# Kernel tuning notes

Hardware: AMD Instinct MI355X
Metric: run time of the kernel (lower is better)

Reference implementation:

```python
import jax, jax.numpy as jnp
import numpy as np

STRIDE = (4, 4)
MASK = (17, 17)
G_MEAN = 85.384
G_STD = 53.798
LEV = 5  # len(bins)
EPS = 1e-8
_BINS = np.array([0.0, 0.5, G_MEAN - G_STD, G_MEAN, G_MEAN + G_STD], dtype=np.float32)
_DISTS = [1, 2, 4]
_THETAS = [0.0, np.pi / 4, np.pi / 2, 3 * np.pi / 4]
# skimage greycomatrix offsets: (row, col) = (round(sin(t)*d), round(cos(t)*d)), dist-major
OFFSETS = [(int(round(np.sin(t) * d)), int(round(np.cos(t) * d))) for d in _DISTS for t in _THETAS]


def setup_inputs():
    key = jax.random.key(0)
    x = jax.random.uniform(key, (8, 1, 512, 512), dtype=jnp.float32) * 255.0
    return {"inputs": x}


def _sliding_windows(x):
    B, C, H, W = x.shape
    nx = (H - MASK[0]) // STRIDE[0] + 1
    ny = (W - MASK[1]) // STRIDE[1] + 1
    rows = (jnp.arange(nx) * STRIDE[0])[:, None] + jnp.arange(MASK[0])  # (nx, Mx)
    cols = (jnp.arange(ny) * STRIDE[1])[:, None] + jnp.arange(MASK[1])  # (ny, My)
    w = x[:, :, rows]              # (B, C, nx, Mx, W)
    w = w[:, :, :, :, cols]        # (B, C, nx, Mx, ny, My)
    return jnp.transpose(w, (0, 1, 2, 4, 3, 5))  # (B, C, nx, ny, Mx, My)


def _statistics(w):
    m = w.mean(axis=(-2, -1))
    s = w.std(axis=(-2, -1))
    mx = w.max(axis=(-2, -1))
    mn = w.min(axis=(-2, -1))
    # Faithful to original: mean is rescaled in-place BEFORE being used in max/min stats
    m = m / G_MEAN
    s = s / G_STD
    mx = (mx - m) / G_STD
    mn = (m - mn) / G_STD
    return jnp.concatenate([m, s, mx, mn], axis=1)  # (B, 4*C, nx, ny)


def _glcm(qf, dr, dc):
    # qf: (Wn, Mx, My) int32 -> normalized symmetric GLCM (Wn, LEV, LEV)
    Mx, My = qf.shape[-2:]
    if dc >= 0:
        a = qf[:, :Mx - dr, :My - dc]
        b = qf[:, dr:, dc:]
    else:
        a = qf[:, :Mx - dr, -dc:]
        b = qf[:, dr:, :My + dc]
    Wn = qf.shape[0]
    code = (a * LEV + b).reshape(Wn, -1)
    flat = (jnp.arange(Wn, dtype=jnp.int32)[:, None] * (LEV * LEV) + code).reshape(-1)
    cnt = jax.ops.segment_sum(jnp.ones(flat.shape, jnp.float32), flat, num_segments=Wn * LEV * LEV)
    G = cnt.reshape(Wn, LEV, LEV)
    G = G + jnp.swapaxes(G, -1, -2)  # symmetric=True
    return G / jnp.sum(G, axis=(-2, -1), keepdims=True)  # normed=True


def _hist_glcm_features(q):
    # q: (B, C, nx, ny, Mx, My) int32 -> (B, 64, nx, ny) (C must be 1)
    B, C, nx, ny, Mx, My = q.shape
    qf = q.reshape(-1, Mx, My)
    Wn = qf.shape[0]
    G = jnp.stack([_glcm(qf, dr, dc) for dr, dc in OFFSETS], axis=1)  # (Wn, 12, L, L)

    I = jnp.arange(LEV, dtype=jnp.float32)
    d2 = (I[:, None] - I[None, :]) ** 2
    contrast = jnp.einsum('wkij,ij->wk', G, d2)
    homogeneity = jnp.einsum('wkij,ij->wk', G, 1.0 / (1.0 + d2))
    energy = jnp.sqrt(jnp.sum(G * G, axis=(-2, -1)))
    Pi = G.sum(axis=-1)   # (Wn, 12, L)
    Pj = G.sum(axis=-2)
    mu_i = jnp.sum(I * Pi, axis=-1)
    mu_j = jnp.sum(I * Pj, axis=-1)
    di = I[None, None, :] - mu_i[..., None]
    dj = I[None, None, :] - mu_j[..., None]
    std_i = jnp.sqrt(jnp.sum(Pi * di * di, axis=-1))
    std_j = jnp.sqrt(jnp.sum(Pj * dj * dj, axis=-1))
    cov = jnp.einsum('wkij,wki,wkj->wk', G, di, dj)
    denom = std_i * std_j
    correlation = jnp.where(denom < 1e-15, 1.0, cov / jnp.maximum(denom, 1e-30))
    entropy = -jnp.sum(G * jnp.log2(G + EPS), axis=(-2, -1))  # (Wn, 12)

    qv = qf.reshape(Wn, -1)
    cnts = jnp.stack([jnp.sum(qv == k, axis=-1) for k in range(1, LEV)], axis=-1).astype(jnp.float32)
    tot = cnts.sum(axis=-1, keepdims=True)
    hist = jnp.where(tot > 0, cnts / jnp.maximum(tot, 1.0), 0.0)  # (Wn, LEV-1)

    feat = jnp.concatenate([hist, contrast, homogeneity, energy, correlation, entropy], axis=-1)
    feat = feat.reshape(B, C, nx, ny, -1)
    return jnp.transpose(feat, (0, 4, 2, 3, 1))[..., 0]  # (B, 64, nx, ny)


def reference(inputs):
    w = _sliding_windows(inputs)                                   # (B,C,nx,ny,17,17)
    stat = _statistics(w)                                          # (B,4,nx,ny)
    q = (jnp.digitize(w, jnp.asarray(_BINS)) - 1).astype(jnp.int32)
    hg = _hist_glcm_features(q)                                    # (B,64,nx,ny)
    feats = jnp.concatenate([stat, hg], axis=1)                    # (B,68,nx,ny)
    return jnp.mean(feats, axis=(-2, -1))                          # (B,68)
```

## Files before the change

kernel.cpp:

```cpp
#include <hip/hip_runtime.h>


#define G_MEAN_F 85.384f
#define G_STD_F  53.798f
#define MASK_WS_BYTES (8u * 512u * 36u * 8u)

__device__ constexpr int LO15[15] = {0,0,0,0,0,1,1,1,1,2,2,2,3,3,4};
__device__ constexpr int HI15[15] = {0,1,2,3,4,1,2,3,4,2,3,4,3,4,4};

__device__ __forceinline__ float wred(float v) {
#pragma unroll
  for (int m = 32; m; m >>= 1) v += __shfl_xor(v, m, 64);
  return v;
}

__device__ __forceinline__ void load_row(const unsigned long long* mrow, int ly4, unsigned m[5]) {
  unsigned long long a = mrow[0], b = mrow[1], c = mrow[2], d = mrow[3];
  m[1] = (unsigned)(a >> ly4) & 0x1FFFFu;
  m[2] = (unsigned)(b >> ly4) & 0x1FFFFu;
  m[3] = (unsigned)(c >> ly4) & 0x1FFFFu;
  m[4] = (unsigned)(d >> ly4) & 0x1FFFFu;
  m[0] = 0x1FFFFu & ~(m[1] | m[2] | m[3] | m[4]);
}

__device__ __forceinline__ void upd(unsigned cnt[15], const unsigned a[5], const unsigned b[5]) {
#pragma unroll
  for (int u = 0; u < 15; ++u) {
    const int i = LO15[u], j = HI15[u];
    unsigned t = a[i] & b[j];
    if (i != j) t |= a[j] & b[i];
    cnt[u] += __popc(t);
  }
}

template<int DR, int DC>
__device__ __forceinline__ void row_pair(unsigned cnt[15], const unsigned long long* mk,
                                         int row, int ly4) {
  unsigned a[5], b[5];
  load_row(mk + row * 5, ly4, a);
  if (DR > 0) load_row(mk + (row + DR) * 5, ly4, b);
  unsigned as[5], bs[5];
#pragma unroll
  for (int v = 0; v < 5; ++v) {
    unsigned bb = (DR > 0) ? b[v] : a[v];
    as[v] = (DC < 0) ? (a[v] >> (-DC)) : a[v];
    bs[v] = (DC > 0) ? (bb >> DC) : bb;
  }
  upd(cnt, as, bs);
}

__device__ __forceinline__ void feat5(const unsigned cnt[15], float Np,
                                      float& con, float& hom, float& ene,
                                      float& corr, float& ent) {
  const float invN = 1.0f / Np;
  const float inv2N = 0.5f / Np;
  con = 0.0f; hom = 0.0f; ent = 0.0f;
  float eac = 0.0f;
  float P[5] = {0, 0, 0, 0, 0};
#pragma unroll
  for (int u = 0; u < 15; ++u) {
    const int lo = LO15[u], hi = HI15[u];
    const float m = (float)cnt[u];
    const float d2 = (float)((hi - lo) * (hi - lo));
    con += m * d2;
    hom += m * (1.0f / (1.0f + d2));
    if (lo == hi) {
      eac += m * m;
      P[lo] += 2.0f * m;
      float g = m * invN;
      ent -= g * __log2f(g + 1e-8f);
    } else {
      eac += 0.5f * m * m;
      P[lo] += m; P[hi] += m;
      float g = m * inv2N;
      ent -= 2.0f * g * __log2f(g + 1e-8f);
    }
  }
  con *= invN;
  hom *= invN;
  ene = sqrtf(eac) * invN;
  float mu = 0.0f;
#pragma unroll
  for (int i = 0; i < 5; ++i) { P[i] *= inv2N; mu += (float)i * P[i]; }
  float s2 = 0.0f;
#pragma unroll
  for (int i = 0; i < 5; ++i) { float d = (float)i - mu; s2 = fmaf(P[i] * d, d, s2); }
  float denom = s2;
  float cov = 0.0f;
#pragma unroll
  for (int u = 0; u < 15; ++u)
    cov += ((float)cnt[u] * invN) * ((float)LO15[u] - mu) * ((float)HI15[u] - mu);
  corr = (denom < 1e-15f) ? 1.0f : cov / fmaxf(denom, 1e-30f);
}

__device__ __forceinline__ void emit2(const unsigned c1[15], const unsigned c2[15], float Np,
                                      bool v1, bool v2, float* pt0, int k0, int k1) {
  float con1, hom1, ene1, cor1, ent1, con2, hom2, ene2, cor2, ent2;
  feat5(c1, Np, con1, hom1, ene1, cor1, ent1);
  feat5(c2, Np, con2, hom2, ene2, cor2, ent2);
  if (!v1) { con1 = 0; hom1 = 0; ene1 = 0; cor1 = 0; ent1 = 0; }
  if (!v2) { con2 = 0; hom2 = 0; ene2 = 0; cor2 = 0; ent2 = 0; }
  float con = wred(con1 + con2), hom = wred(hom1 + hom2), ene = wred(ene1 + ene2);
  float cor = wred(cor1 + cor2), ent = wred(ent1 + ent2);
  if ((threadIdx.x & 63) == 0) {
    const float s = 1.0f / 15376.0f;
    pt0[(8 + k0) * 128] = con * s;
    pt0[(20 + k0) * 128] = hom * s;
    pt0[(32 + k0) * 128] = ene * s;
    pt0[(44 + k0) * 128] = cor * s;
    pt0[(56 + k0) * 128] = ent * s;
    if (k1 >= 0) {
      pt0[(8 + k1) * 128] = con * s;
      pt0[(20 + k1) * 128] = hom * s;
      pt0[(32 + k1) * 128] = ene * s;
      pt0[(44 + k1) * 128] = cor * s;
      pt0[(56 + k1) * 128] = ent * s;
    }
  }
}

template<int DR, int DC>
__device__ __forceinline__ void glcm_pass(const unsigned long long* mk, int s, int ly4,
                                          float Np, bool v1, bool v2, float* pt0,
                                          int k0, int k1) {
  unsigned A[15], S[15], B[15];
#pragma unroll
  for (int u = 0; u < 15; ++u) { A[u] = 0; S[u] = 0; B[u] = 0; }
#pragma unroll 1
  for (int R = 0; R < 4; ++R) row_pair<DR, DC>(A, mk, s + R, ly4);
#pragma unroll 1
  for (int R = 4; R < 17 - DR; ++R) row_pair<DR, DC>(S, mk, s + R, ly4);
#pragma unroll 1
  for (int R = 17 - DR; R < 21 - DR; ++R) row_pair<DR, DC>(B, mk, s + R, ly4);
#pragma unroll
  for (int u = 0; u < 15; ++u) { A[u] += S[u]; B[u] += S[u]; }
  emit2(A, B, Np, v1, v2, pt0, k0, k1);
}

__global__ __launch_bounds__(64)
void mask_build_kernel(const float* __restrict__ x, unsigned long long* __restrict__ mg) {
  const int lane = threadIdx.x;
  const int r = blockIdx.x;
  const int b = blockIdx.y;
  const float* xr = x + ((size_t)b * 512 + r) * 512;
  unsigned long long* mr = mg + ((size_t)b * 512 + r) * 36;

  const float T1 = 0.5f;
  const float T2 = (float)(85.384 - 53.798);
  const float T3 = 85.384f;
  const float T4 = (float)(85.384 + 53.798);

#pragma unroll 1
  for (int seg = 0; seg < 8; ++seg) {
    float xv = xr[seg * 64 + lane];
    int q = (int)(xv >= T1) + (int)(xv >= T2) + (int)(xv >= T3) + (int)(xv >= T4);
    unsigned long long b1 = __ballot(q == 1);
    unsigned long long b2 = __ballot(q == 2);
    unsigned long long b3 = __ballot(q == 3);
    unsigned long long b4 = __ballot(q == 4);
    if (lane < 4) {
      unsigned long long bv = (lane == 0) ? b1 : (lane == 1) ? b2 : (lane == 2) ? b3 : b4;
      mr[seg * 4 + lane] = bv;
    }
  }
  if (lane < 4) mr[32 + lane] = 0;
}

__global__ __launch_bounds__(128)
void glcm_feat_kernel(const float* __restrict__ x,
                      const unsigned long long* __restrict__ mg,
                      float* __restrict__ part) {
  __shared__ unsigned long long masks[77 * 5];

  const int tid = threadIdx.x;
  const int lane = tid & 63;
  const int wid = tid >> 6;
  const int role = blockIdx.x >> 4;
  const int ty = blockIdx.x & 15;
  const int tx = blockIdx.y;
  const int b = blockIdx.z;
  const int px0 = tx * 64;
  const int py0 = ty * 32;
  const float* xb = x + (size_t)b * 512 * 512;

  const int s0 = py0 >> 6;
  const int sh = py0 & 63;
  const unsigned long long* mgb = mg + (size_t)b * 512 * 36;
#pragma unroll 1
  for (int t = tid; t < 77 * 4; t += 128) {
    int row = t >> 2, lev = t & 3;
    int gr = px0 + row; if (gr > 511) gr = 511;
    const unsigned long long* p = mgb + (size_t)gr * 36 + s0 * 4 + lev;
    unsigned long long w0 = p[0];
    unsigned long long w1 = p[4];
    masks[row * 5 + lev] = sh ? ((w0 >> 32) | (w1 << 32)) : w0;
  }
  __syncthreads();

  const int lxp = lane >> 3, ly = lane & 7;
  const int wx1 = tx * 16 + 2 * lxp;
  const int wy = ty * 8 + ly;
  const bool vy = (wy < 124);
  const bool v1 = (wx1 < 124) && vy;
  const bool v2 = (wx1 + 1 < 124) && vy;
  const int s = 8 * lxp;
  const int ly4 = ly * 4;
  const int tile = tx * 16 + ty;
  float* pt0 = part + (size_t)b * 68 * 128 + tile;

  if (role == 0) {
    if (wid == 0) {
      unsigned hA[4] = {0,0,0,0}, hS[4] = {0,0,0,0}, hB[4] = {0,0,0,0};
#pragma unroll 1
      for (int R = 0; R < 21; ++R) {
        unsigned m[5];
        load_row(masks + (s + R) * 5, ly4, m);
        unsigned* h = (R < 4) ? hA : (R < 17) ? hS : hB;
#pragma unroll
        for (int v = 0; v < 4; ++v) h[v] += __popc(m[v + 1]);
      }
      int sp = px0 + s; if (sp > 488) sp = 488;
      int c0 = py0 + ly4; if (c0 > 492) c0 = 492;
      const float* fw = xb + (size_t)sp * 512 + c0;
      float sA = 0, qA = 0, sS = 0, qS = 0, sB = 0, qB = 0;
      float mxA = -1e30f, mnA = 1e30f, mxS = -1e30f, mnS = 1e30f, mxB = -1e30f, mnB = 1e30f;
#pragma unroll 1
      for (int r = 0; r < 21; ++r) {
        const float* p = fw + r * 512;
        const float4* p4 = (const float4*)p;
        float rs = 0, rq = 0, rmx = -1e30f, rmn = 1e30f;
#pragma unroll
        for (int w = 0; w < 4; ++w) {
          float4 f = p4[w];
          rs += f.x; rq = fmaf(f.x, f.x, rq); rmx = fmaxf(rmx, f.x); rmn = fminf(rmn, f.x);
          rs += f.y; rq = fmaf(f.y, f.y, rq); rmx = fmaxf(rmx, f.y); rmn = fminf(rmn, f.y);
          rs += f.z; rq = fmaf(f.z, f.z, rq); rmx = fmaxf(rmx, f.z); rmn = fminf(rmn, f.z);
          rs += f.w; rq = fmaf(f.w, f.w, rq); rmx = fmaxf(rmx, f.w); rmn = fminf(rmn, f.w);
        }
        float t = p[16];
        rs += t; rq = fmaf(t, t, rq); rmx = fmaxf(rmx, t); rmn = fminf(rmn, t);
        if (r < 4)       { sA += rs; qA += rq; mxA = fmaxf(mxA, rmx); mnA = fminf(mnA, rmn); }
        else if (r < 17) { sS += rs; qS += rq; mxS = fmaxf(mxS, rmx); mnS = fminf(mnS, rmn); }
        else             { sB += rs; qB += rq; mxB = fmaxf(mxB, rmx); mnB = fminf(mnB, rmn); }
      }
      float ch[8][2];
#pragma unroll
      for (int w = 0; w < 2; ++w) {
        float sum = w ? (sS + sB) : (sA + sS);
        float ssq = w ? (qS + qB) : (qA + qS);
        float mx = w ? fmaxf(mxS, mxB) : fmaxf(mxA, mxS);
        float mn = w ? fminf(mnS, mnB) : fminf(mnA, mnS);
        unsigned t1 = w ? (hS[0] + hB[0]) : (hA[0] + hS[0]);
        unsigned t2 = w ? (hS[1] + hB[1]) : (hA[1] + hS[1]);
        unsigned t3 = w ? (hS[2] + hB[2]) : (hA[2] + hS[2]);
        unsigned t4 = w ? (hS[3] + hB[3]) : (hA[3] + hS[3]);
        float mean = sum * (1.0f / 289.0f);
        float var = fmaxf(ssq * (1.0f / 289.0f) - mean * mean, 0.0f);
        float fm = mean / G_MEAN_F;
        ch[0][w] = fm;
        ch[1][w] = sqrtf(var) / G_STD_F;
        ch[2][w] = (mx - fm) / G_STD_F;
        ch[3][w] = (fm - mn) / G_STD_F;
        unsigned tot = t1 + t2 + t3 + t4;
        float ti = (tot > 0) ? 1.0f / (float)tot : 0.0f;
        ch[4][w] = (float)t1 * ti;
        ch[5][w] = (float)t2 * ti;
        ch[6][w] = (float)t3 * ti;
        ch[7][w] = (float)t4 * ti;
      }
#pragma unroll
      for (int c = 0; c < 8; ++c) {
        float f = (v1 ? ch[c][0] : 0.0f) + (v2 ? ch[c][1] : 0.0f);
        f = wred(f);
        if (lane == 0) pt0[c * 128] = f * (1.0f / 15376.0f);
      }
    } else {
      glcm_pass<0, 1>(masks, s, ly4, 272.0f, v1, v2, pt0, 0, -1);
      glcm_pass<1, 0>(masks, s, ly4, 272.0f, v1, v2, pt0, 2, -1);
    }
  } else if (role == 1) {
    if (wid == 0) {
      glcm_pass<0, 2>(masks, s, ly4, 255.0f, v1, v2, pt0, 4, -1);
      glcm_pass<1, 1>(masks, s, ly4, 256.0f, v1, v2, pt0, 1, 5);
    } else {
      glcm_pass<0, 4>(masks, s, ly4, 221.0f, v1, v2, pt0, 8, -1);
      glcm_pass<1, -1>(masks, s, ly4, 256.0f, v1, v2, pt0, 3, 7);
    }
  } else {
    if (wid == 0) {
      glcm_pass<2, 0>(masks, s, ly4, 255.0f, v1, v2, pt0, 6, -1);
      glcm_pass<3, 3>(masks, s, ly4, 196.0f, v1, v2, pt0, 9, -1);
    } else {
      glcm_pass<4, 0>(masks, s, ly4, 221.0f, v1, v2, pt0, 10, -1);
      glcm_pass<3, -3>(masks, s, ly4, 196.0f, v1, v2, pt0, 11, -1);
    }
  }
}

__global__ __launch_bounds__(64)
void reduce_kernel(const float* __restrict__ part, float* __restrict__ out) {
  const int ch = blockIdx.x;
  const int b = blockIdx.y;
  const int lane = threadIdx.x;
  const float2* p = (const float2*)(part + ((size_t)b * 68 + ch) * 128);
  float2 f = p[lane];
  float v = f.x + f.y;
  v = wred(v);
  if (lane == 0) out[b * 68 + ch] = v;
}

extern "C" void kernel_launch(void* const* d_in, const int* in_sizes, int n_in,
                              void* d_out, int out_size, void* d_ws, size_t ws_size,
                              hipStream_t stream)
{
  const float* x = (const float*)d_in[0];
  float* out = (float*)d_out;
  unsigned long long* mg = (unsigned long long*)d_ws;
  float* part = (float*)((char*)d_ws + MASK_WS_BYTES);

  mask_build_kernel<<<dim3(512, 8), dim3(64), 0, stream>>>(x, mg);
  glcm_feat_kernel<<<dim3(48, 8, 8), dim3(128), 0, stream>>>(x, mg, part);
  reduce_kernel<<<dim3(68, 8), dim3(64), 0, stream>>>(part, out);
}
```

Measured before the change: 114.3 us.

## Split GLCM work into one pass per wave and reuse loaded mask rows

Doubles the grid so each wave runs a single GLCM offset pass instead of two, and moves the histogram counting off the statistics wave onto a separate wave. Row-offset passes now keep a small register ring of previously loaded rows, so each mask row is read from LDS once rather than twice. This targets per-wave serial latency and duplicate LDS loads, at the cost of staging the mask tile into shared memory twice as many times and using more registers for the row ring.

```diff
diff --git a/kernel.cpp b/kernel.cpp
--- a/kernel.cpp
+++ b/kernel.cpp
@@ -23,30 +23,21 @@
   m[0] = 0x1FFFFu & ~(m[1] | m[2] | m[3] | m[4]);
 }
 
-__device__ __forceinline__ void upd(unsigned cnt[15], const unsigned a[5], const unsigned b[5]) {
+template<int DC>
+__device__ __forceinline__ void updoff(unsigned cnt[15], const unsigned a[5], const unsigned b[5]) {
+  unsigned as[5], bs[5];
+#pragma unroll
+  for (int v = 0; v < 5; ++v) {
+    as[v] = (DC < 0) ? (a[v] >> (-DC)) : a[v];
+    bs[v] = (DC > 0) ? (b[v] >> DC) : b[v];
+  }
 #pragma unroll
   for (int u = 0; u < 15; ++u) {
     const int i = LO15[u], j = HI15[u];
-    unsigned t = a[i] & b[j];
-    if (i != j) t |= a[j] & b[i];
+    unsigned t = as[i] & bs[j];
+    if (i != j) t |= as[j] & bs[i];
     cnt[u] += __popc(t);
   }
-}
-
-template<int DR, int DC>
-__device__ __forceinline__ void row_pair(unsigned cnt[15], const unsigned long long* mk,
-                                         int row, int ly4) {
-  unsigned a[5], b[5];
-  load_row(mk + row * 5, ly4, a);
-  if (DR > 0) load_row(mk + (row + DR) * 5, ly4, b);
-  unsigned as[5], bs[5];
-#pragma unroll
-  for (int v = 0; v < 5; ++v) {
-    unsigned bb = (DR > 0) ? b[v] : a[v];
-    as[v] = (DC < 0) ? (a[v] >> (-DC)) : a[v];
-    bs[v] = (DC > 0) ? (bb >> DC) : bb;
-  }
-  upd(cnt, as, bs);
 }
 
 __device__ __forceinline__ void feat5(const unsigned cnt[15], float Np,
@@ -119,6 +110,16 @@
   }
 }
 
+template<int DR>
+__device__ __forceinline__ void shiftbuf(unsigned buf[][5], const unsigned c[5]) {
+#pragma unroll
+  for (int i = 0; i < DR - 1; ++i)
+#pragma unroll
+    for (int v = 0; v < 5; ++v) buf[i][v] = buf[i + 1][v];
+#pragma unroll
+  for (int v = 0; v < 5; ++v) buf[DR - 1][v] = c[v];
+}
+
 template<int DR, int DC>
 __device__ __forceinline__ void glcm_pass(const unsigned long long* mk, int s, int ly4,
                                           float Np, bool v1, bool v2, float* pt0,
@@ -126,12 +127,37 @@
   unsigned A[15], S[15], B[15];
 #pragma unroll
   for (int u = 0; u < 15; ++u) { A[u] = 0; S[u] = 0; B[u] = 0; }
-#pragma unroll 1
-  for (int R = 0; R < 4; ++R) row_pair<DR, DC>(A, mk, s + R, ly4);
-#pragma unroll 1
-  for (int R = 4; R < 17 - DR; ++R) row_pair<DR, DC>(S, mk, s + R, ly4);
-#pragma unroll 1
-  for (int R = 17 - DR; R < 21 - DR; ++R) row_pair<DR, DC>(B, mk, s + R, ly4);
+  unsigned c[5];
+  if (DR == 0) {
+#pragma unroll 1
+    for (int R = 0; R < 4; ++R)  { load_row(mk + (s + R) * 5, ly4, c); updoff<DC>(A, c, c); }
+#pragma unroll 1
+    for (int R = 4; R < 17; ++R) { load_row(mk + (s + R) * 5, ly4, c); updoff<DC>(S, c, c); }
+#pragma unroll 1
+    for (int R = 17; R < 21; ++R){ load_row(mk + (s + R) * 5, ly4, c); updoff<DC>(B, c, c); }
+  } else {
+    unsigned buf[DR > 0 ? DR : 1][5];
+#pragma unroll
+    for (int i = 0; i < DR; ++i) load_row(mk + (s + i) * 5, ly4, buf[i]);
+#pragma unroll 1
+    for (int R = 0; R < 4; ++R) {
+      load_row(mk + (s + R + DR) * 5, ly4, c);
+      updoff<DC>(A, buf[0], c);
+      shiftbuf<DR>(buf, c);
+    }
+#pragma unroll 1
+    for (int R = 4; R < 17 - DR; ++R) {
+      load_row(mk + (s + R + DR) * 5, ly4, c);
+      updoff<DC>(S, buf[0], c);
+      shiftbuf<DR>(buf, c);
+    }
+#pragma unroll 1
+    for (int R = 17 - DR; R < 21 - DR; ++R) {
+      load_row(mk + (s + R + DR) * 5, ly4, c);
+      updoff<DC>(B, buf[0], c);
+      shiftbuf<DR>(buf, c);
+    }
+  }
 #pragma unroll
   for (int u = 0; u < 15; ++u) { A[u] += S[u]; B[u] += S[u]; }
   emit2(A, B, Np, v1, v2, pt0, k0, k1);
@@ -175,7 +201,7 @@
   const int tid = threadIdx.x;
   const int lane = tid & 63;
   const int wid = tid >> 6;
-  const int role = blockIdx.x >> 4;
+  const int u = blockIdx.x >> 4;
   const int ty = blockIdx.x & 15;
   const int tx = blockIdx.y;
   const int b = blockIdx.z;
@@ -208,17 +234,8 @@
   const int tile = tx * 16 + ty;
   float* pt0 = part + (size_t)b * 68 * 128 + tile;
 
-  if (role == 0) {
+  if (u == 0) {
     if (wid == 0) {
-      unsigned hA[4] = {0,0,0,0}, hS[4] = {0,0,0,0}, hB[4] = {0,0,0,0};
-#pragma unroll 1
-      for (int R = 0; R < 21; ++R) {
-        unsigned m[5];
-        load_row(masks + (s + R) * 5, ly4, m);
-        unsigned* h = (R < 4) ? hA : (R < 17) ? hS : hB;
-#pragma unroll
-        for (int v = 0; v < 4; ++v) h[v] += __popc(m[v + 1]);
-      }
       int sp = px0 + s; if (sp > 488) sp = 488;
       int c0 = py0 + ly4; if (c0 > 492) c0 = 492;
       const float* fw = xb + (size_t)sp * 512 + c0;
@@ -243,17 +260,13 @@
         else if (r < 17) { sS += rs; qS += rq; mxS = fmaxf(mxS, rmx); mnS = fminf(mnS, rmn); }
         else             { sB += rs; qB += rq; mxB = fmaxf(mxB, rmx); mnB = fminf(mnB, rmn); }
       }
-      float ch[8][2];
+      float ch[4][2];
 #pragma unroll
       for (int w = 0; w < 2; ++w) {
         float sum = w ? (sS + sB) : (sA + sS);
         float ssq = w ? (qS + qB) : (qA + qS);
         float mx = w ? fmaxf(mxS, mxB) : fmaxf(mxA, mxS);
         float mn = w ? fminf(mnS, mnB) : fminf(mnA, mnS);
-        unsigned t1 = w ? (hS[0] + hB[0]) : (hA[0] + hS[0]);
-        unsigned t2 = w ? (hS[1] + hB[1]) : (hA[1] + hS[1]);
-        unsigned t3 = w ? (hS[2] + hB[2]) : (hA[2] + hS[2]);
-        unsigned t4 = w ? (hS[3] + hB[3]) : (hA[3] + hS[3]);
         float mean = sum * (1.0f / 289.0f);
         float var = fmaxf(ssq * (1.0f / 289.0f) - mean * mean, 0.0f);
         float fm = mean / G_MEAN_F;
@@ -261,39 +274,59 @@
         ch[1][w] = sqrtf(var) / G_STD_F;
         ch[2][w] = (mx - fm) / G_STD_F;
         ch[3][w] = (fm - mn) / G_STD_F;
-        unsigned tot = t1 + t2 + t3 + t4;
-        float ti = (tot > 0) ? 1.0f / (float)tot : 0.0f;
-        ch[4][w] = (float)t1 * ti;
-        ch[5][w] = (float)t2 * ti;
-        ch[6][w] = (float)t3 * ti;
-        ch[7][w] = (float)t4 * ti;
-      }
-#pragma unroll
-      for (int c = 0; c < 8; ++c) {
+      }
+#pragma unroll
+      for (int c = 0; c < 4; ++c) {
         float f = (v1 ? ch[c][0] : 0.0f) + (v2 ? ch[c][1] : 0.0f);
         f = wred(f);
         if (lane == 0) pt0[c * 128] = f * (1.0f / 15376.0f);
       }
     } else {
-      glcm_pass<0, 1>(masks, s, ly4, 272.0f, v1, v2, pt0, 0, -1);
-      glcm_pass<1, 0>(masks, s, ly4, 272.0f, v1, v2, pt0, 2, -1);
-    }
-  } else if (role == 1) {
-    if (wid == 0) {
-      glcm_pass<0, 2>(masks, s, ly4, 255.0f, v1, v2, pt0, 4, -1);
-      glcm_pass<1, 1>(masks, s, ly4, 256.0f, v1, v2, pt0, 1, 5);
-    } else {
-      glcm_pass<0, 4>(masks, s, ly4, 221.0f, v1, v2, pt0, 8, -1);
-      glcm_pass<1, -1>(masks, s, ly4, 256.0f, v1, v2, pt0, 3, 7);
-    }
+      unsigned hA[4] = {0,0,0,0}, hS[4] = {0,0,0,0}, hB[4] = {0,0,0,0};
+#pragma unroll 1
+      for (int R = 0; R < 21; ++R) {
+        unsigned m[5];
+        load_row(masks + (s + R) * 5, ly4, m);
+        unsigned* h = (R < 4) ? hA : (R < 17) ? hS : hB;
+#pragma unroll
+        for (int v = 0; v < 4; ++v) h[v] += __popc(m[v + 1]);
+      }
+      float ch[4][2];
+#pragma unroll
+      for (int w = 0; w < 2; ++w) {
+        unsigned t1 = w ? (hS[0] + hB[0]) : (hA[0] + hS[0]);
+        unsigned t2 = w ? (hS[1] + hB[1]) : (hA[1] + hS[1]);
+        unsigned t3 = w ? (hS[2] + hB[2]) : (hA[2] + hS[2]);
+        unsigned t4 = w ? (hS[3] + hB[3]) : (hA[3] + hS[3]);
+        unsigned tot = t1 + t2 + t3 + t4;
+        float ti = (tot > 0) ? 1.0f / (float)tot : 0.0f;
+        ch[0][w] = (float)t1 * ti;
+        ch[1][w] = (float)t2 * ti;
+        ch[2][w] = (float)t3 * ti;
+        ch[3][w] = (float)t4 * ti;
+      }
+#pragma unroll
+      for (int c = 0; c < 4; ++c) {
+        float f = (v1 ? ch[c][0] : 0.0f) + (v2 ? ch[c][1] : 0.0f);
+        f = wred(f);
+        if (lane == 0) pt0[(4 + c) * 128] = f * (1.0f / 15376.0f);
+      }
+    }
+  } else if (u == 1) {
+    if (wid == 0) glcm_pass<0, 1>(masks, s, ly4, 272.0f, v1, v2, pt0, 0, -1);
+    else          glcm_pass<1, 0>(masks, s, ly4, 272.0f, v1, v2, pt0, 2, -1);
+  } else if (u == 2) {
+    if (wid == 0) glcm_pass<0, 2>(masks, s, ly4, 255.0f, v1, v2, pt0, 4, -1);
+    else          glcm_pass<1, 1>(masks, s, ly4, 256.0f, v1, v2, pt0, 1, 5);
+  } else if (u == 3) {
+    if (wid == 0) glcm_pass<0, 4>(masks, s, ly4, 221.0f, v1, v2, pt0, 8, -1);
+    else          glcm_pass<1, -1>(masks, s, ly4, 256.0f, v1, v2, pt0, 3, 7);
+  } else if (u == 4) {
+    if (wid == 0) glcm_pass<2, 0>(masks, s, ly4, 255.0f, v1, v2, pt0, 6, -1);
+    else          glcm_pass<3, 3>(masks, s, ly4, 196.0f, v1, v2, pt0, 9, -1);
   } else {
-    if (wid == 0) {
-      glcm_pass<2, 0>(masks, s, ly4, 255.0f, v1, v2, pt0, 6, -1);
-      glcm_pass<3, 3>(masks, s, ly4, 196.0f, v1, v2, pt0, 9, -1);
-    } else {
-      glcm_pass<4, 0>(masks, s, ly4, 221.0f, v1, v2, pt0, 10, -1);
-      glcm_pass<3, -3>(masks, s, ly4, 196.0f, v1, v2, pt0, 11, -1);
-    }
+    if (wid == 0) glcm_pass<4, 0>(masks, s, ly4, 221.0f, v1, v2, pt0, 10, -1);
+    else          glcm_pass<3, -3>(masks, s, ly4, 196.0f, v1, v2, pt0, 11, -1);
   }
 }
 
@@ -319,6 +352,6 @@
   float* part = (float*)((char*)d_ws + MASK_WS_BYTES);
 
   mask_build_kernel<<<dim3(512, 8), dim3(64), 0, stream>>>(x, mg);
-  glcm_feat_kernel<<<dim3(48, 8, 8), dim3(128), 0, stream>>>(x, mg, part);
+  glcm_feat_kernel<<<dim3(96, 8, 8), dim3(128), 0, stream>>>(x, mg, part);
   reduce_kernel<<<dim3(68, 8), dim3(64), 0, stream>>>(part, out);
 }
```

New measurement: 113.4 us. About the same (-0.7%).
